# Kernel tuning notes

Measured on AMD Instinct MI355X. Metric: run time of the kernel, lower is better.

Reference implementation:

```python
import jax, jax.numpy as jnp
import numpy as np
from jax import lax

EPS = 1e-07
B, NPRIM, NSEC, DP, DS = 512, 1152, 10, 8, 16


def setup_inputs() -> dict:
    key = jax.random.key(0)
    ks = jax.random.split(key, 12)
    inp = {}
    inp['x'] = jax.random.uniform(ks[0], (B, 28, 28, 1), dtype=jnp.float32)
    inp['labels'] = jax.random.randint(ks[1], (B,), 0, NSEC)
    # conv1: 9x9, 1 -> 256, relu ; conv2 (primary caps): 9x9 stride2, 256 -> 256
    inp['conv1_k'] = jax.random.normal(ks[2], (9, 9, 1, 256), dtype=jnp.float32) * 0.05
    inp['conv1_b'] = jnp.zeros((256,), dtype=jnp.float32)
    inp['conv2_k'] = jax.random.normal(ks[3], (9, 9, 256, 256), dtype=jnp.float32) * 0.02
    inp['conv2_b'] = jnp.zeros((256,), dtype=jnp.float32)
    # pose transform W: [1152, 10, 16, 8]
    inp['w'] = jax.random.normal(ks[4], (NPRIM, NSEC, DS, DP), dtype=jnp.float32) * 0.05
    # decoder
    inp['d1_w'] = jax.random.normal(ks[5], (NSEC * DS, 512), dtype=jnp.float32) * 0.05
    inp['d1_b'] = jnp.zeros((512,), dtype=jnp.float32)
    inp['d2_w'] = jax.random.normal(ks[6], (512, 1024), dtype=jnp.float32) * 0.05
    inp['d2_b'] = jnp.zeros((1024,), dtype=jnp.float32)
    inp['d3_w'] = jax.random.normal(ks[7], (1024, 784), dtype=jnp.float32) * 0.05
    inp['d3_b'] = jnp.zeros((784,), dtype=jnp.float32)
    return inp


def _conv(x, k, b, stride):
    y = lax.conv_general_dilated(x, k, (stride, stride), 'VALID',
                                 dimension_numbers=('NHWC', 'HWIO', 'NHWC'))
    return y + b


def _squash(s):
    # s: [..., D]
    s_norm = jnp.linalg.norm(s, axis=-1, keepdims=True)
    sq = jnp.square(s_norm)
    return sq / (1.0 + sq) * s / (s_norm + EPS)


def reference(x, labels, conv1_k, conv1_b, conv2_k, conv2_b, w,
              d1_w, d1_b, d2_w, d2_b, d3_w, d3_b):
    h = jax.nn.relu(_conv(x, conv1_k, conv1_b, 1))        # [B,20,20,256]
    p = _conv(h, conv2_k, conv2_b, 2)                      # [B,6,6,256]
    u = p.reshape(x.shape[0], NPRIM, DP)                   # [B,1152,8]
    # u_hat[b,n,s,d] = sum_p w[n,s,d,p] * u[b,n,p]
    u_hat = jnp.einsum('nsdp,bnp->bnsd', w, u)             # [B,1152,10,16]

    b_logits = jnp.zeros((x.shape[0], NPRIM, NSEC, 1), dtype=u_hat.dtype)
    v = None
    for _ in range(3):  # r routing iterations (fixed, small)
        c = jax.nn.softmax(b_logits, axis=-2)              # softmax over 10 secondary caps
        s = jnp.sum(c * u_hat, axis=1, keepdims=True)      # [B,1,10,16]
        v = _squash(s)                                     # [B,1,10,16]
        agreement = jnp.sum(u_hat * v, axis=-1, keepdims=True)  # [B,1152,10,1]
        b_logits = b_logits + agreement

    y = jax.nn.one_hot(labels, NSEC, dtype=v.dtype)        # [B,10]
    mask = y[:, None, :, None]                             # [B,1,10,1]
    v_masked = mask * v
    v_flat = v_masked.reshape(-1, NSEC * DS)               # [B,160]
    r1 = jax.nn.relu(v_flat @ d1_w + d1_b)
    r2 = jax.nn.relu(r1 @ d2_w + d2_b)
    recon = jax.nn.sigmoid(r2 @ d3_w + d3_b)               # [B,784]
    return v, recon
```

## Files before the change

### kernel.cpp

```cpp
#include <hip/hip_runtime.h>

#define USH unsigned short

__device__ inline float bf2f(USH u){ return __uint_as_float(((unsigned)u)<<16); }
__device__ inline USH f2bf(float f){
  unsigned u = __float_as_uint(f);
  return (USH)((u + 0x7FFFu + ((u>>16)&1u))>>16);
}

typedef __attribute__((ext_vector_type(8))) short bf16x8;
typedef __attribute__((ext_vector_type(4))) float f32x4;

__device__ inline void gll16(const USH* g, USH* l){
  __builtin_amdgcn_global_load_lds((const __attribute__((address_space(1))) void*)g,
                                   (__attribute__((address_space(3))) void*)l, 16, 0, 0);
}

__global__ __launch_bounds__(256) void im2col_k(
    const float* __restrict__ x, USH* __restrict__ xcol)
{
  int b = blockIdx.x, t = threadIdx.x;
  __shared__ float xs[784];
  for (int i = t; i < 784; i += 256) xs[i] = x[b*784 + i];
  __syncthreads();
  USH* dst = xcol + (size_t)b*38400;
  for (int idx = t; idx < 38400; idx += 256) {
    int sp = idx / 96, k = idx - sp*96;
    int y = sp / 20, xx = sp - y*20;
    USH v = 0;
    if (k < 81) {
      int dy = k / 9, dx = k - dy*9;
      v = f2bf(xs[(y+dy)*28 + xx + dx]);
    }
    dst[idx] = v;
  }
}

__global__ __launch_bounds__(256) void tr_k1(const float* __restrict__ k1, USH* __restrict__ k1T)
{
  int n = threadIdx.x;
  for (int k = 0; k < 96; ++k)
    k1T[n*96 + k] = (k < 81) ? f2bf(k1[k*256 + n]) : (USH)0;
}

__global__ __launch_bounds__(256) void gemm1(
    const USH* __restrict__ xcol, const USH* __restrict__ k1T,
    const float* __restrict__ b1, USH* __restrict__ h)
{
  int t = threadIdx.x;
  int m0 = blockIdx.x * 64;
  int lane = t & 63, wave = t >> 6;
  int wn = wave * 64;
  int fr = lane & 15, fq = lane >> 4;

  f32x4 acc[4][4];
#pragma unroll
  for (int i = 0; i < 4; ++i)
#pragma unroll
    for (int j = 0; j < 4; ++j)
#pragma unroll
      for (int r = 0; r < 4; ++r) acc[i][j][r] = 0.f;

#pragma unroll
  for (int kt = 0; kt < 3; ++kt) {
    int kc = kt*32 + fq*8;
    bf16x8 af[4], bg[4];
#pragma unroll
    for (int mf = 0; mf < 4; ++mf)
      af[mf] = *(const bf16x8*)&xcol[(size_t)(m0 + mf*16 + fr)*96 + kc];
#pragma unroll
    for (int nf = 0; nf < 4; ++nf)
      bg[nf] = *(const bf16x8*)&k1T[(size_t)(wn + nf*16 + fr)*96 + kc];
#pragma unroll
    for (int mf = 0; mf < 4; ++mf)
#pragma unroll
      for (int nf = 0; nf < 4; ++nf)
        acc[mf][nf] = __builtin_amdgcn_mfma_f32_16x16x32_bf16(af[mf], bg[nf], acc[mf][nf], 0,0,0);
  }

#pragma unroll
  for (int mf = 0; mf < 4; ++mf)
#pragma unroll
    for (int nf = 0; nf < 4; ++nf) {
      int n = wn + nf*16 + fr;
      float bias = b1[n];
#pragma unroll
      for (int r = 0; r < 4; ++r) {
        int m = m0 + mf*16 + fq*4 + r;
        float v = acc[mf][nf][r] + bias;
        h[(size_t)m*256 + n] = f2bf(v > 0.f ? v : 0.f);
      }
    }
}

__global__ __launch_bounds__(256) void tr_k2(const float* __restrict__ k2, USH* __restrict__ k2T)
{
  __shared__ float tile[32][33];
  int kb = blockIdx.x*32, nb = blockIdx.y*32;
  int tx = threadIdx.x & 31, ty = threadIdx.x >> 5;
#pragma unroll
  for (int r = 0; r < 4; ++r) {
    int k = kb + ty + r*8;
    tile[ty + r*8][tx] = k2[(size_t)k*256 + nb + tx];
  }
  __syncthreads();
#pragma unroll
  for (int r = 0; r < 4; ++r) {
    int n = nb + ty + r*8;
    k2T[(size_t)n*20736 + kb + tx] = f2bf(tile[tx][ty + r*8]);
  }
}

__global__ __launch_bounds__(256) void conv2_mfma(
    const USH* __restrict__ h, const USH* __restrict__ k2T,
    float* __restrict__ up)
{
  __shared__ __align__(16) USH Asm[2][128*64];
  __shared__ __align__(16) USH Bsm[2][64*64];
  int t = threadIdx.x;
  int flat = blockIdx.x;
  int xcd  = flat & 7;
  int slot = flat >> 3;
  int nb   = slot & 3;
  int rest = slot >> 2;
  int mb_l = rest % 18;
  int ksl  = rest / 18;
  int mb   = xcd*18 + mb_l;

  int sg = (((t&7) ^ ((t>>3)&7)) << 3);

  int arow_off[4];
#pragma unroll
  for (int i = 0; i < 4; ++i) {
    int row = (t>>3) + i*32;
    int m = mb*128 + row;
    int bb = m/36, r = m - bb*36;
    int oy = r/6, ox = r - oy*6;
    arow_off[i] = bb*102400 + oy*10240 + ox*512 + sg;
  }
  int brow_off[2];
#pragma unroll
  for (int i = 0; i < 2; ++i) {
    int nl = (t>>3) + i*32;
    brow_off[i] = (nb*64 + nl)*20736 + sg;
  }

  int lane = t & 63;
  int wave = t >> 6;
  int wm = (wave>>1)*64, wn = (wave&1)*32;
  int fr = lane & 15, fq = lane >> 4;

  f32x4 acc[4][2];
#pragma unroll
  for (int i = 0; i < 4; ++i)
#pragma unroll
    for (int j = 0; j < 2; ++j)
#pragma unroll
      for (int r = 0; r < 4; ++r) acc[i][j][r] = 0.f;

  int rg0 = (((0*4 + fq) ^ (fr&7)) << 3);
  int rg1 = (((1*4 + fq) ^ (fr&7)) << 3);

#define STAGE(buf, kt) do {                                            \
    int j_ = (kt) >> 2;                                                \
    int cin0_ = ((kt) & 3) << 6;                                       \
    int dy_ = j_/9, dx_ = j_ - dy_*9;                                  \
    int koff_ = (dy_*20 + dx_)*256 + cin0_;                            \
    USH* Ad_ = &Asm[buf][(t>>6)*512];                                  \
    USH* Bd_ = &Bsm[buf][(t>>6)*512];                                  \
    _Pragma("unroll")                                                  \
    for (int i_ = 0; i_ < 4; ++i_) gll16(h + arow_off[i_] + koff_, Ad_ + i_*2048); \
    _Pragma("unroll")                                                  \
    for (int i_ = 0; i_ < 2; ++i_) gll16(k2T + brow_off[i_] + (kt)*64, Bd_ + i_*2048); \
  } while(0)

  const int k0 = ksl*81, kend = k0 + 81;
  STAGE(0, k0);
  __syncthreads();

  int cur = 0;
  for (int kt = k0; kt < kend; ++kt) {
    if (kt + 1 < kend) STAGE(cur^1, kt+1);

    bf16x8 af[4][2], bg[2][2];
#pragma unroll
    for (int mf = 0; mf < 4; ++mf) {
      af[mf][0] = *(const bf16x8*)&Asm[cur][(wm + mf*16 + fr)*64 + rg0];
      af[mf][1] = *(const bf16x8*)&Asm[cur][(wm + mf*16 + fr)*64 + rg1];
    }
#pragma unroll
    for (int nf = 0; nf < 2; ++nf) {
      bg[nf][0] = *(const bf16x8*)&Bsm[cur][(wn + nf*16 + fr)*64 + rg0];
      bg[nf][1] = *(const bf16x8*)&Bsm[cur][(wn + nf*16 + fr)*64 + rg1];
    }
#pragma unroll
    for (int mf = 0; mf < 4; ++mf)
#pragma unroll
      for (int nf = 0; nf < 2; ++nf) {
        acc[mf][nf] = __builtin_amdgcn_mfma_f32_16x16x32_bf16(af[mf][0], bg[nf][0], acc[mf][nf], 0,0,0);
        acc[mf][nf] = __builtin_amdgcn_mfma_f32_16x16x32_bf16(af[mf][1], bg[nf][1], acc[mf][nf], 0,0,0);
      }
    __syncthreads();
    cur ^= 1;
  }
#undef STAGE

  float* dst = up + (size_t)ksl*4718592;
#pragma unroll
  for (int mf = 0; mf < 4; ++mf)
#pragma unroll
    for (int nf = 0; nf < 2; ++nf) {
      int n = nb*64 + wn + nf*16 + fr;
#pragma unroll
      for (int r = 0; r < 4; ++r) {
        int m = mb*128 + wm + mf*16 + fq*4 + r;
        dst[(size_t)m*256 + n] = acc[mf][nf][r];
      }
    }
}

__global__ __launch_bounds__(256) void reduce_u(
    const float* __restrict__ up, const float* __restrict__ b2, float* __restrict__ u)
{
  int i = blockIdx.x*256 + threadIdx.x;
  f32x4 a = *(const f32x4*)&up[(size_t)i*4];
  f32x4 b = *(const f32x4*)&up[4718592ull + (size_t)i*4];
  f32x4 c = *(const f32x4*)&up[9437184ull + (size_t)i*4];
  f32x4 d = *(const f32x4*)&up[14155776ull + (size_t)i*4];
  int n0 = (i*4) & 255;
  f32x4 o;
#pragma unroll
  for (int j = 0; j < 4; ++j) o[j] = (a[j] + b[j]) + (c[j] + d[j]) + b2[n0 + j];
  *(f32x4*)&u[(size_t)i*4] = o;
}

__global__ __launch_bounds__(192) void wsum_tr(const float* __restrict__ w,
    float* __restrict__ Ws)
{
  int n = blockIdx.x, t = threadIdx.x;
  __shared__ float wn[1280];
  for (int i = t; i < 1280; i += 192) wn[i] = w[n*1280 + i];
  __syncthreads();
  if (t < 160) {
#pragma unroll
    for (int p = 0; p < 8; ++p)
      Ws[((size_t)n*8 + p)*160 + t] = wn[(t>>4)*128 + (t&15)*8 + p];
  }
}

__global__ __launch_bounds__(192) void p1gemm(const float* __restrict__ u,
    const float* __restrict__ Ws, float* __restrict__ part)
{
  int b0 = blockIdx.x*32, k0 = blockIdx.y*288;
  int t = threadIdx.x;
  __shared__ float usm[288*36];
  for (int i = t; i < 288*32; i += 192) {
    int bl = i/288, kk = i - bl*288;
    usm[kk*36 + bl] = u[(size_t)(b0+bl)*9216 + k0 + kk];
  }
  __syncthreads();
  if (t < 160) {
    const float* wp = Ws + (size_t)k0*160 + t;
#pragma unroll 1
    for (int half = 0; half < 2; ++half) {
      float acc[16];
#pragma unroll
      for (int i = 0; i < 16; ++i) acc[i] = 0.f;
      for (int kk = 0; kk < 288; ++kk) {
        float wv = wp[(size_t)kk*160];
        const f32x4* ub = (const f32x4*)&usm[kk*36 + half*16];
        f32x4 u0 = ub[0], u1 = ub[1], u2 = ub[2], u3 = ub[3];
#pragma unroll
        for (int i = 0; i < 4; ++i) {
          acc[i]    += u0[i]*wv;
          acc[4+i]  += u1[i]*wv;
          acc[8+i]  += u2[i]*wv;
          acc[12+i] += u3[i]*wv;
        }
      }
      float* pp = &part[((size_t)blockIdx.y*512 + b0 + half*16)*160 + t];
#pragma unroll
      for (int i = 0; i < 16; ++i) pp[(size_t)i*160] = acc[i];
    }
  }
}

__global__ __launch_bounds__(192) void squash1(const float* __restrict__ part,
    float* __restrict__ vout)
{
  int b = blockIdx.x, t = threadIdx.x;
  if (t < 160) {
    float sv = 0.f;
    for (int ks = 0; ks < 32; ++ks) sv += part[((size_t)ks*512 + b)*160 + t];
    sv *= 0.1f;
    float n2 = sv*sv;
    n2 += __shfl_xor(n2, 1, 16);
    n2 += __shfl_xor(n2, 2, 16);
    n2 += __shfl_xor(n2, 4, 16);
    n2 += __shfl_xor(n2, 8, 16);
    float nrm = sqrtf(n2);
    float o = (n2/(1.f + n2)) * sv / (nrm + 1e-7f);
    vout[b*160 + t] = o;
  }
}

__global__ __launch_bounds__(256) void uhat_kernel(
    const float* __restrict__ u, const float* __restrict__ w, USH* __restrict__ uh)
{
  int n = blockIdx.x, b0 = blockIdx.y*64;
  int t = threadIdx.x;
  __shared__ float wsm[20*65];
  __shared__ float usm[512];
  for (int i = t; i < 1280; i += 256) wsm[(i>>6)*65 + (i&63)] = w[n*1280 + i];
  for (int i = t; i < 512; i += 256) {
    int bl = i>>3, p = i&7;
    usm[i] = u[(size_t)(b0+bl)*9216 + n*8 + p];
  }
  __syncthreads();
  USH* dst = uh + ((size_t)n*512 + b0)*160;
  for (int v = t; v < 1280; v += 256) {
    int bl = v/20, oct = v - bl*20;
    const float* upt = &usm[bl*8];
    bf16x8 pk;
#pragma unroll
    for (int j = 0; j < 8; ++j) {
      const float* wp = &wsm[oct*65 + j*8];
      float a = 0.f;
#pragma unroll
      for (int p = 0; p < 8; ++p) a += wp[p]*upt[p];
      pk[j] = (short)f2bf(a);
    }
    *(bf16x8*)&dst[(size_t)v*8] = pk;
  }
}

__global__ __launch_bounds__(256) void route_part(
    const USH* __restrict__ uh, const float* __restrict__ vin,
    float* __restrict__ partR)
{
  int b = blockIdx.x, nc = blockIdx.y;
  int t = threadIdx.x;
  int lane = t & 63, w = t >> 6;
  int grp = lane >> 4, s = lane & 15;
  int stream = w*4 + grp;
  bool act = s < 10;

  float vr[16];
  {
    const float* vp = vin + b*160 + s*16;
#pragma unroll
    for (int d = 0; d < 16; ++d) vr[d] = act ? vp[d] : 0.f;
  }
  float acc[16];
#pragma unroll
  for (int d = 0; d < 16; ++d) acc[d] = 0.f;

  int nbase = nc*288 + stream*18;
  const USH* base = uh + ((size_t)nbase*512 + b)*160 + s*16;
  const size_t nstride = (size_t)512*160;

  bf16x8 c0{}, c1{};
  if (act) { c0 = *(const bf16x8*)base; c1 = *(const bf16x8*)(base + 8); }

  for (int ni = 0; ni < 18; ++ni) {
    bf16x8 f0 = c0, f1 = c1;
    if (ni + 1 < 18 && act) {
      const USH* p = base + (size_t)(ni+1)*nstride;
      f0 = *(const bf16x8*)p;
      f1 = *(const bf16x8*)(p + 8);
    }
    float uv[16];
    if (act) {
#pragma unroll
      for (int d = 0; d < 8; ++d) { uv[d] = bf2f((USH)c0[d]); uv[8+d] = bf2f((USH)c1[d]); }
    } else {
#pragma unroll
      for (int d = 0; d < 16; ++d) uv[d] = 0.f;
    }
    c0 = f0; c1 = f1;

    float dot = 0.f;
#pragma unroll
    for (int d = 0; d < 16; ++d) dot += uv[d]*vr[d];
    float lg = act ? dot : -1e30f;
    float mx = lg;
    mx = fmaxf(mx, __shfl_xor(mx, 1, 16));
    mx = fmaxf(mx, __shfl_xor(mx, 2, 16));
    mx = fmaxf(mx, __shfl_xor(mx, 4, 16));
    mx = fmaxf(mx, __shfl_xor(mx, 8, 16));
    float e = __expf(lg - mx);
    float sum = e;
    sum += __shfl_xor(sum, 1, 16);
    sum += __shfl_xor(sum, 2, 16);
    sum += __shfl_xor(sum, 4, 16);
    sum += __shfl_xor(sum, 8, 16);
    float c = e / sum;
#pragma unroll
    for (int d = 0; d < 16; ++d) acc[d] += c*uv[d];
  }

  __shared__ float red[16][168];
  if (act) {
#pragma unroll
    for (int d = 0; d < 16; ++d) red[stream][s*16 + d] = acc[d];
  }
  __syncthreads();
  if (t < 160) {
    float sv = 0.f;
#pragma unroll
    for (int k = 0; k < 16; ++k) sv += red[k][t];
    partR[((size_t)nc*512 + b)*160 + t] = sv;
  }
}

template<int PASS>
__global__ __launch_bounds__(192) void squash_part(const float* __restrict__ partR,
    const float* __restrict__ vprev, float* __restrict__ vout, float* __restrict__ vext)
{
  int b = blockIdx.x, t = threadIdx.x;
  if (t < 160) {
    float sv = 0.f;
#pragma unroll
    for (int nc = 0; nc < 4; ++nc) sv += partR[((size_t)nc*512 + b)*160 + t];
    float n2 = sv*sv;
    n2 += __shfl_xor(n2, 1, 16);
    n2 += __shfl_xor(n2, 2, 16);
    n2 += __shfl_xor(n2, 4, 16);
    n2 += __shfl_xor(n2, 8, 16);
    float nrm = sqrtf(n2);
    float o = (n2/(1.f + n2)) * sv / (nrm + 1e-7f);
    vout[b*160 + t] = o;
    if (PASS == 2) vext[b*160 + t] = vprev[b*160 + t] + o;
    if (PASS == 3) vext[b*160 + t] = o;
  }
}

__global__ __launch_bounds__(512) void d1_kernel(const float* __restrict__ v3,
    const int* __restrict__ labels, const float* __restrict__ w,
    const float* __restrict__ bias, float* __restrict__ r1)
{
  int b = blockIdx.x; int j = threadIdx.x;
  int lb = labels[b];
  float acc = bias[j];
#pragma unroll
  for (int d = 0; d < 16; ++d)
    acc += v3[b*160 + lb*16 + d] * w[(lb*16 + d)*512 + j];
  r1[(size_t)b*512 + j] = acc > 0.f ? acc : 0.f;
}

__global__ __launch_bounds__(256) void d2_kernel(const float* __restrict__ a,
    const float* __restrict__ w, const float* __restrict__ bias, float* __restrict__ o)
{
  int j = blockIdx.x*256 + threadIdx.x;
  int b0 = blockIdx.y*4;
  __shared__ float as[4*512];
  for (int i = threadIdx.x; i < 4*512; i += 256) as[i] = a[(size_t)(b0 + (i>>9))*512 + (i&511)];
  __syncthreads();
  float acc[4];
  float bs = bias[j];
#pragma unroll
  for (int i = 0; i < 4; ++i) acc[i] = bs;
  for (int k = 0; k < 512; ++k) {
    float wv = w[(size_t)k*1024 + j];
#pragma unroll
    for (int i = 0; i < 4; ++i) acc[i] += as[i*512 + k]*wv;
  }
#pragma unroll
  for (int i = 0; i < 4; ++i)
    o[(size_t)(b0+i)*1024 + j] = acc[i] > 0.f ? acc[i] : 0.f;
}

__global__ __launch_bounds__(256) void d3_kernel(const float* __restrict__ a,
    const float* __restrict__ w, const float* __restrict__ bias, float* __restrict__ o)
{
  int j = blockIdx.x*256 + threadIdx.x;
  int b0 = blockIdx.y*4;
  __shared__ float as[4*1024];
  for (int i = threadIdx.x; i < 4*1024; i += 256) as[i] = a[(size_t)(b0 + (i>>10))*1024 + (i&1023)];
  __syncthreads();
  if (j < 784) {
    float acc[4];
    float bs = bias[j];
#pragma unroll
    for (int i = 0; i < 4; ++i) acc[i] = bs;
    for (int k = 0; k < 1024; ++k) {
      float wv = w[(size_t)k*784 + j];
#pragma unroll
      for (int i = 0; i < 4; ++i) acc[i] += as[i*1024 + k]*wv;
    }
#pragma unroll
    for (int i = 0; i < 4; ++i)
      o[(size_t)(b0+i)*784 + j] = 1.f/(1.f + __expf(-acc[i]));
  }
}

extern "C" void kernel_launch(void* const* d_in, const int* in_sizes, int n_in,
                              void* d_out, int out_size, void* d_ws, size_t ws_size,
                              hipStream_t stream)
{
  const float* x   = (const float*)d_in[0];
  const int*   lab = (const int*)  d_in[1];
  const float* k1  = (const float*)d_in[2];
  const float* b1  = (const float*)d_in[3];
  const float* k2  = (const float*)d_in[4];
  const float* b2  = (const float*)d_in[5];
  const float* w   = (const float*)d_in[6];
  const float* d1w = (const float*)d_in[7];
  const float* d1b = (const float*)d_in[8];
  const float* d2w = (const float*)d_in[9];
  const float* d2b = (const float*)d_in[10];
  const float* d3w = (const float*)d_in[11];
  const float* d3b = (const float*)d_in[12];
  float* out = (float*)d_out;

  char* ws = (char*)d_ws;
  USH*   uh    = (USH*)(ws + 0);
  USH*   h     = (USH*)(ws + 0);
  float* up    = (float*)(ws + 104857600ull);
  USH*   xcol  = (USH*)(ws + 142606336ull);
  float* u     = (float*)(ws + 188743680ull);
  USH*   k2T   = (USH*)(ws + 207618048ull);
  float* part  = (float*)(ws + 207618048ull);
  float* partR = (float*)(ws + 207618048ull);
  float* Wsum  = (float*)(ws + 218234880ull);
  USH*   k1T   = (USH*)(ws + 241827840ull);
  float* v1    = (float*)(ws + 242155520ull);
  float* v2    = (float*)(ws + 242483200ull);
  float* v3    = (float*)(ws + 242810880ull);
  float* vsum  = (float*)(ws + 243138560ull);
  float* r1    = (float*)(ws + 243466240ull);
  float* r2    = (float*)(ws + 244514816ull);

  im2col_k<<<512, 256, 0, stream>>>(x, xcol);
  tr_k1<<<1, 256, 0, stream>>>(k1, k1T);
  gemm1<<<3200, 256, 0, stream>>>(xcol, k1T, b1, h);

  tr_k2<<<dim3(648,8), 256, 0, stream>>>(k2, k2T);
  conv2_mfma<<<2304, 256, 0, stream>>>(h, k2T, up);
  reduce_u<<<4608, 256, 0, stream>>>(up, b2, u);

  wsum_tr<<<1152, 192, 0, stream>>>(w, Wsum);
  p1gemm<<<dim3(16,32), 192, 0, stream>>>(u, Wsum, part);
  squash1<<<512, 192, 0, stream>>>(part, v1);

  uhat_kernel<<<dim3(1152,8), 256, 0, stream>>>(u, w, uh);

  route_part<<<dim3(512,4), 256, 0, stream>>>(uh, v1, partR);
  squash_part<2><<<512, 192, 0, stream>>>(partR, v1, v2, vsum);
  route_part<<<dim3(512,4), 256, 0, stream>>>(uh, vsum, partR);
  squash_part<3><<<512, 192, 0, stream>>>(partR, nullptr, v3, out);

  d1_kernel<<<512, 512, 0, stream>>>(v3, lab, d1w, d1b, r1);
  d2_kernel<<<dim3(4,128), 256, 0, stream>>>(r1, d2w, d2b, r2);
  d3_kernel<<<dim3(4,128), 256, 0, stream>>>(r2, d3w, d3b, out + 81920);
}
```

Measured before the change: 618.6 us.

## Remap route_part blocks to batch×primary tiles for coalesced u_hat reads

Each route_part block now covers 16 batch rows and 16 primary capsules, so adjacent threads read contiguous 320-byte batch rows of u_hat instead of each wavefront striding across primary capsules for a single batch row. The shared-memory reduction and its barrier are gone; each thread writes its own partial vector with vector stores. In exchange there are 72 partial slices instead of 4, so squash_part must sum 72 partials per element and the partial buffer grows. The workspace layout is shuffled so the larger buffer fits.

```diff
diff --git a/kernel.cpp b/kernel.cpp
--- a/kernel.cpp
+++ b/kernel.cpp
@@ -338,33 +338,34 @@
     const USH* __restrict__ uh, const float* __restrict__ vin,
     float* __restrict__ partR)
 {
-  int b = blockIdx.x, nc = blockIdx.y;
+  int bc = blockIdx.x, nc = blockIdx.y;
+  int b0 = bc*16, n0 = nc*16;
   int t = threadIdx.x;
-  int lane = t & 63, w = t >> 6;
-  int grp = lane >> 4, s = lane & 15;
-  int stream = w*4 + grp;
+  int bL = t >> 4, s = t & 15;
   bool act = s < 10;
+  int b = b0 + bL;
 
   float vr[16];
-  {
-    const float* vp = vin + b*160 + s*16;
-#pragma unroll
-    for (int d = 0; d < 16; ++d) vr[d] = act ? vp[d] : 0.f;
+#pragma unroll
+  for (int d = 0; d < 16; ++d) vr[d] = 0.f;
+  if (act) {
+    const float* vp = vin + (size_t)b*160 + s*16;
+#pragma unroll
+    for (int d = 0; d < 16; ++d) vr[d] = vp[d];
   }
   float acc[16];
 #pragma unroll
   for (int d = 0; d < 16; ++d) acc[d] = 0.f;
 
-  int nbase = nc*288 + stream*18;
-  const USH* base = uh + ((size_t)nbase*512 + b)*160 + s*16;
   const size_t nstride = (size_t)512*160;
+  const USH* base = uh + ((size_t)n0*512 + b)*160 + s*16;
 
   bf16x8 c0{}, c1{};
   if (act) { c0 = *(const bf16x8*)base; c1 = *(const bf16x8*)(base + 8); }
 
-  for (int ni = 0; ni < 18; ++ni) {
+  for (int ni = 0; ni < 16; ++ni) {
     bf16x8 f0 = c0, f1 = c1;
-    if (ni + 1 < 18 && act) {
+    if (ni + 1 < 16 && act) {
       const USH* p = base + (size_t)(ni+1)*nstride;
       f0 = *(const bf16x8*)p;
       f1 = *(const bf16x8*)(p + 8);
@@ -399,17 +400,15 @@
     for (int d = 0; d < 16; ++d) acc[d] += c*uv[d];
   }
 
-  __shared__ float red[16][168];
   if (act) {
-#pragma unroll
-    for (int d = 0; d < 16; ++d) red[stream][s*16 + d] = acc[d];
-  }
-  __syncthreads();
-  if (t < 160) {
-    float sv = 0.f;
-#pragma unroll
-    for (int k = 0; k < 16; ++k) sv += red[k][t];
-    partR[((size_t)nc*512 + b)*160 + t] = sv;
+    float* pp = &partR[((size_t)nc*512 + b)*160 + s*16];
+#pragma unroll
+    for (int q = 0; q < 4; ++q) {
+      f32x4 o;
+#pragma unroll
+      for (int j = 0; j < 4; ++j) o[j] = acc[q*4 + j];
+      *(f32x4*)(pp + q*4) = o;
+    }
   }
 }
 
@@ -420,8 +419,7 @@
   int b = blockIdx.x, t = threadIdx.x;
   if (t < 160) {
     float sv = 0.f;
-#pragma unroll
-    for (int nc = 0; nc < 4; ++nc) sv += partR[((size_t)nc*512 + b)*160 + t];
+    for (int nc = 0; nc < 72; ++nc) sv += partR[((size_t)nc*512 + b)*160 + t];
     float n2 = sv*sv;
     n2 += __shfl_xor(n2, 1, 16);
     n2 += __shfl_xor(n2, 2, 16);
@@ -520,9 +518,9 @@
   USH*   xcol  = (USH*)(ws + 142606336ull);
   float* u     = (float*)(ws + 188743680ull);
   USH*   k2T   = (USH*)(ws + 207618048ull);
-  float* part  = (float*)(ws + 207618048ull);
-  float* partR = (float*)(ws + 207618048ull);
-  float* Wsum  = (float*)(ws + 218234880ull);
+  float* Wsum  = (float*)(ws + 207618048ull);
+  float* part  = (float*)(ws + 218234880ull);
+  float* partR = (float*)(ws + 218234880ull);
   USH*   k1T   = (USH*)(ws + 241827840ull);
   float* v1    = (float*)(ws + 242155520ull);
   float* v2    = (float*)(ws + 242483200ull);
@@ -545,9 +543,9 @@
 
   uhat_kernel<<<dim3(1152,8), 256, 0, stream>>>(u, w, uh);
 
-  route_part<<<dim3(512,4), 256, 0, stream>>>(uh, v1, partR);
+  route_part<<<dim3(32,72), 256, 0, stream>>>(uh, v1, partR);
   squash_part<2><<<512, 192, 0, stream>>>(partR, v1, v2, vsum);
-  route_part<<<dim3(512,4), 256, 0, stream>>>(uh, vsum, partR);
+  route_part<<<dim3(32,72), 256, 0, stream>>>(uh, vsum, partR);
   squash_part<3><<<512, 192, 0, stream>>>(partR, nullptr, v3, out);
 
   d1_kernel<<<512, 512, 0, stream>>>(v3, lab, d1w, d1b, r1);
```

Result: no change. 629.5 us (+1.8%).
